# Performance work log

Hardware: AMD Instinct MI355X
Metric: run time of the kernel (lower is better)

## Reference

```python
import jax, jax.numpy as jnp
import numpy as np

K = 2            # top-k experts per sample
LOSS_COEF = 0.01


def _cv_squared(v):
    eps = 1e-10
    return jnp.var(v, ddof=1) / (jnp.mean(v) ** 2 + eps)


def setup_inputs() -> dict:
    key = jax.random.key(0)
    k1, k2, k3, k4 = jax.random.split(key, 4)
    B, S, D, O, E = 32, 512, 768, 768, 8
    return {
        "x": jax.random.normal(k1, (B, S, D), dtype=jnp.float32),
        "w_gate": jax.random.normal(k2, (D, E), dtype=jnp.float32) * 0.02,
        "weight": jax.random.normal(k3, (E, O, D), dtype=jnp.float32) * 0.02,
        "bias": jax.random.normal(k4, (E, O), dtype=jnp.float32) * 0.02,
    }


def reference(x, w_gate, weight, bias):
    # x: [B, S, D]; w_gate: [D, E]; weight: [E, O, D]; bias: [E, O]
    B = x.shape[0]
    E = w_gate.shape[1]

    # --- top-k gating (eval mode: clean logits, no noise) ---
    pooled = x.mean(-2)                       # [B, D] (moe_level != 'task'/'token')
    logits = pooled @ w_gate                  # [B, E]
    top_vals, top_idx = jax.lax.top_k(logits, min(K + 1, E))
    tk_vals, tk_idx = top_vals[:, :K], top_idx[:, :K]
    tk_gates = jax.nn.softmax(tk_vals, axis=1)            # [B, K]
    gates = jnp.zeros_like(logits).at[jnp.arange(B)[:, None], tk_idx].set(tk_gates)  # [B, E]

    load = (gates > 0).sum(0).astype(jnp.float32)          # [E]
    importance = gates.sum(0)                              # [E]
    loss = (_cv_squared(importance) + _cv_squared(load)) * LOSS_COEF

    # --- per-sample soft combination of expert weights, then batched linear ---
    # same math as sum_e gates[b,e] * weight[e] without materializing [B,E,O,D]
    expert_w = jnp.einsum('be,eoi->boi', gates, weight)    # [B, O, D]
    expert_b = jnp.einsum('be,eo->bo', gates, bias)        # [B, O]
    y = jnp.einsum('bij,bkj->bik', x, expert_w) + expert_b[:, None, :]  # [B, S, O]
    return (y, loss)
```

## Files before the change

kernel.cpp:

```cpp
#include <hip/hip_runtime.h>
#include <hip/hip_bf16.h>
#include <stdint.h>

#define B_ 32
#define S_ 512
#define D_ 768
#define O_ 768
#define E_ 8
#define YSIZE (B_ * S_ * O_)
#define BK 32

typedef __attribute__((ext_vector_type(8))) short bf16x8;
typedef __attribute__((ext_vector_type(4))) float f32x4;

static __device__ __forceinline__ unsigned short f2bf(float f) {
  union { float f; uint32_t u; } v; v.f = f;
  uint32_t u = v.u;
  uint32_t r = u + 0x7fff + ((u >> 16) & 1);
  return (unsigned short)(r >> 16);
}

static __device__ __forceinline__ void async_load16(const void* g, void* l) {
  __builtin_amdgcn_global_load_lds(
      (const __attribute__((address_space(1))) void*)g,
      (__attribute__((address_space(3))) void*)l, 16, 0, 0);
}

__global__ void k_pool_convert(const float* __restrict__ x,
                               unsigned short* __restrict__ xb,
                               float* __restrict__ psum) {
  int d  = blockIdx.x * 256 + threadIdx.x;
  int b  = blockIdx.y;
  int sc = blockIdx.z;
  const float* xp = x + ((size_t)(b * S_ + sc * 128)) * D_ + d;
  unsigned short* op = xb + ((size_t)(b * S_ + sc * 128)) * D_ + d;
  float sum = 0.f;
  #pragma unroll 8
  for (int s = 0; s < 128; ++s) {
    float v = xp[(size_t)s * D_];
    sum += v;
    op[(size_t)s * D_] = f2bf(v);
  }
  psum[(sc * B_ + b) * D_ + d] = sum;
}

__global__ __launch_bounds__(256) void k_logits(
    const float* __restrict__ psum, const float* __restrict__ w_gate,
    float* __restrict__ gates, int* __restrict__ eidx,
    float* __restrict__ gval) {
  int b = blockIdx.x;
  int tid = threadIdx.x;
  float acc[E_];
  #pragma unroll
  for (int e = 0; e < E_; ++e) acc[e] = 0.f;

  for (int d = tid; d < D_; d += 256) {
    float pooled = (psum[b * D_ + d] + psum[(B_ + b) * D_ + d] +
                    psum[(2 * B_ + b) * D_ + d] + psum[(3 * B_ + b) * D_ + d]) *
                   (1.0f / (float)S_);
    const float* wg = w_gate + d * E_;
    #pragma unroll
    for (int e = 0; e < E_; ++e) acc[e] += pooled * wg[e];
  }
  #pragma unroll
  for (int off = 32; off > 0; off >>= 1) {
    #pragma unroll
    for (int e = 0; e < E_; ++e) acc[e] += __shfl_down(acc[e], off, 64);
  }
  __shared__ float part[4][E_];
  if ((tid & 63) == 0) {
    #pragma unroll
    for (int e = 0; e < E_; ++e) part[tid >> 6][e] = acc[e];
  }
  __syncthreads();
  if (tid == 0) {
    float lg[E_];
    #pragma unroll
    for (int e = 0; e < E_; ++e)
      lg[e] = part[0][e] + part[1][e] + part[2][e] + part[3][e];
    int i0 = 0; float v0 = lg[0];
    #pragma unroll
    for (int e = 1; e < E_; ++e) { if (lg[e] > v0) { v0 = lg[e]; i0 = e; } }
    int i1 = -1; float v1 = -1e30f;
    #pragma unroll
    for (int e = 0; e < E_; ++e) {
      if (e == i0) continue;
      if (lg[e] > v1) { v1 = lg[e]; i1 = e; }
    }
    float m  = fmaxf(v0, v1);
    float x0 = expf(v0 - m), x1 = expf(v1 - m);
    float s  = x0 + x1;
    float g0 = x0 / s, g1 = x1 / s;
    #pragma unroll
    for (int e = 0; e < E_; ++e)
      gates[b * E_ + e] = (e == i0) ? g0 : ((e == i1) ? g1 : 0.f);
    eidx[b] = i0; eidx[B_ + b] = i1;
    gval[b] = g0; gval[B_ + b] = g1;
  }
}

__global__ void k_loss(const float* __restrict__ gates,
                       float* __restrict__ loss_out) {
  int tid = threadIdx.x;
  __shared__ float imp[E_], loadv[E_];
  if (tid < E_) {
    float s = 0.f, c = 0.f;
    for (int b = 0; b < B_; ++b) {
      float g = gates[b * E_ + tid];
      s += g;
      c += (g > 0.f) ? 1.f : 0.f;
    }
    imp[tid] = s; loadv[tid] = c;
  }
  __syncthreads();
  if (tid == 0) {
    double mi = 0, ml = 0;
    for (int e = 0; e < E_; ++e) { mi += imp[e]; ml += loadv[e]; }
    mi /= E_; ml /= E_;
    double vi = 0, vl = 0;
    for (int e = 0; e < E_; ++e) {
      double di = imp[e] - mi, dl = loadv[e] - ml;
      vi += di * di; vl += dl * dl;
    }
    vi /= (E_ - 1); vl /= (E_ - 1);
    double cvi = vi / (mi * mi + 1e-10);
    double cvl = vl / (ml * ml + 1e-10);
    loss_out[0] = (float)((cvi + cvl) * 0.01);
  }
}

__global__ __launch_bounds__(256) void k_moe_gemm(
    const unsigned short* __restrict__ xb, const float* __restrict__ weight,
    const int* __restrict__ eidx, const float* __restrict__ gval,
    const float* __restrict__ bias, float* __restrict__ y) {
  __shared__ unsigned short Alds[128 * BK];
  __shared__ unsigned short Blds[128 * BK];

  int b    = blockIdx.y;
  int tile = blockIdx.x;
  int st = tile & 3;
  int ot = tile >> 2;
  int s0 = st * 128, o0 = ot * 128;

  int tid  = threadIdx.x;
  int wave = tid >> 6, lane = tid & 63;
  int wm = wave & 1, wn = wave >> 1;

  int   e0 = eidx[b], e1 = eidx[B_ + b];
  float g0 = gval[b], g1 = gval[B_ + b];

  const unsigned short* Abase = xb + ((size_t)(b * S_ + s0)) * D_;
  const float* W0 = weight + (size_t)e0 * O_ * D_ + (size_t)o0 * D_;
  const float* W1 = weight + (size_t)e1 * O_ * D_ + (size_t)o0 * D_;

  int brow  = tid >> 1;
  int bhalf = tid & 1;

  f32x4 acc[4][4];
  #pragma unroll
  for (int i = 0; i < 4; ++i)
    #pragma unroll
    for (int j = 0; j < 4; ++j) acc[i][j] = (f32x4){0.f, 0.f, 0.f, 0.f};

  int a_chunk0 = wave * 2;
  int a_r = lane >> 2;
  int a_c = (lane & 3) * 8;

  for (int kk = 0; kk < D_; kk += BK) {
    __syncthreads();
    #pragma unroll
    for (int j = 0; j < 2; ++j) {
      int chunk = a_chunk0 + j;
      const unsigned short* src =
          Abase + (size_t)(chunk * 16 + a_r) * D_ + kk + a_c;
      async_load16(src, Alds + chunk * 512);
    }
    {
      const float* p0 = W0 + (size_t)brow * D_ + kk + bhalf * 16;
      const float* p1 = W1 + (size_t)brow * D_ + kk + bhalf * 16;
      uint32_t pk[8];
      #pragma unroll
      for (int i = 0; i < 4; ++i) {
        float4 u0 = ((const float4*)p0)[i];
        float4 u1 = ((const float4*)p1)[i];
        float c0 = g0 * u0.x + g1 * u1.x;
        float c1 = g0 * u0.y + g1 * u1.y;
        float c2 = g0 * u0.z + g1 * u1.z;
        float c3 = g0 * u0.w + g1 * u1.w;
        pk[i * 2 + 0] = (uint32_t)f2bf(c0) | ((uint32_t)f2bf(c1) << 16);
        pk[i * 2 + 1] = (uint32_t)f2bf(c2) | ((uint32_t)f2bf(c3) << 16);
      }
      uint32_t* dst = (uint32_t*)(Blds + brow * 32 + bhalf * 16);
      ((uint4*)dst)[0] = make_uint4(pk[0], pk[1], pk[2], pk[3]);
      ((uint4*)dst)[1] = make_uint4(pk[4], pk[5], pk[6], pk[7]);
    }
    __syncthreads();

    bf16x8 af[4], bfr[4];
    int koff = (lane >> 4) * 8;
    int r16  = lane & 15;
    #pragma unroll
    for (int mi = 0; mi < 4; ++mi)
      af[mi] = *(const bf16x8*)(Alds + (wm * 64 + mi * 16 + r16) * BK + koff);
    #pragma unroll
    for (int ni = 0; ni < 4; ++ni)
      bfr[ni] = *(const bf16x8*)(Blds + (wn * 64 + ni * 16 + r16) * BK + koff);
    #pragma unroll
    for (int mi = 0; mi < 4; ++mi)
      #pragma unroll
      for (int ni = 0; ni < 4; ++ni)
        acc[mi][ni] = __builtin_amdgcn_mfma_f32_16x16x32_bf16(
            af[mi], bfr[ni], acc[mi][ni], 0, 0, 0);
  }

  float* Y = y + ((size_t)(b * S_ + s0)) * O_ + o0;
  int col   = lane & 15;
  int rquad = (lane >> 4) * 4;
  #pragma unroll
  for (int ni = 0; ni < 4; ++ni) {
    int n = wn * 64 + ni * 16 + col;
    float cbv = g0 * bias[e0 * O_ + o0 + n] + g1 * bias[e1 * O_ + o0 + n];
    #pragma unroll
    for (int mi = 0; mi < 4; ++mi) {
      #pragma unroll
      for (int r = 0; r < 4; ++r) {
        int m = wm * 64 + mi * 16 + rquad + r;
        Y[(size_t)m * O_ + n] = acc[mi][ni][r] + cbv;
      }
    }
  }
}

extern "C" void kernel_launch(void* const* d_in, const int* in_sizes, int n_in,
                              void* d_out, int out_size, void* d_ws, size_t ws_size,
                              hipStream_t stream) {
  const float* x      = (const float*)d_in[0];
  const float* w_gate = (const float*)d_in[1];
  const float* weight = (const float*)d_in[2];
  const float* bias   = (const float*)d_in[3];
  float* y = (float*)d_out;

  float* psum  = (float*)d_ws;
  float* gates = psum + 4 * B_ * D_;
  int*   eidx  = (int*)(gates + B_ * E_);
  float* gval  = (float*)(eidx + 64);
  unsigned short* xb = (unsigned short*)((char*)d_ws + 524288);

  k_pool_convert<<<dim3(3, 32, 4), 256, 0, stream>>>(x, xb, psum);
  k_logits<<<32, 256, 0, stream>>>(psum, w_gate, gates, eidx, gval);
  k_loss<<<1, 64, 0, stream>>>(gates, y + YSIZE);
  k_moe_gemm<<<dim3(24, 32), 256, 0, stream>>>(xb, weight, eidx, gval, bias, y);
}
```

Baseline: 191.9 us.

## Precombine per-sample expert weights to bf16 and async-load both GEMM operands

Adds a k_combine kernel that reads all 8 expert weight slices once and writes a gated bf16 combined weight matrix per sample to workspace. The GEMM then loads B tiles with async global-to-LDS copies like A, instead of redundantly reading two fp32 expert slices and mixing them in every tile. Pool/convert is also split into more blocks (16 sequence chunks) for more parallelism. The cost is an extra kernel launch plus writing and rereading about 37 MB of combined weights.

Result: faster. 181.2 us (-5.6%).

```diff
diff --git a/kernel.cpp b/kernel.cpp
--- a/kernel.cpp
+++ b/kernel.cpp
@@ -9,6 +9,7 @@
 #define E_ 8
 #define YSIZE (B_ * S_ * O_)
 #define BK 32
+#define WSLICE (O_ * D_)
 
 typedef __attribute__((ext_vector_type(8))) short bf16x8;
 typedef __attribute__((ext_vector_type(4))) float f32x4;
@@ -32,11 +33,11 @@
   int d  = blockIdx.x * 256 + threadIdx.x;
   int b  = blockIdx.y;
   int sc = blockIdx.z;
-  const float* xp = x + ((size_t)(b * S_ + sc * 128)) * D_ + d;
-  unsigned short* op = xb + ((size_t)(b * S_ + sc * 128)) * D_ + d;
+  const float* xp = x + ((size_t)(b * S_ + sc * 32)) * D_ + d;
+  unsigned short* op = xb + ((size_t)(b * S_ + sc * 32)) * D_ + d;
   float sum = 0.f;
   #pragma unroll 8
-  for (int s = 0; s < 128; ++s) {
+  for (int s = 0; s < 32; ++s) {
     float v = xp[(size_t)s * D_];
     sum += v;
     op[(size_t)s * D_] = f2bf(v);
@@ -55,12 +56,13 @@
   for (int e = 0; e < E_; ++e) acc[e] = 0.f;
 
   for (int d = tid; d < D_; d += 256) {
-    float pooled = (psum[b * D_ + d] + psum[(B_ + b) * D_ + d] +
-                    psum[(2 * B_ + b) * D_ + d] + psum[(3 * B_ + b) * D_ + d]) *
-                   (1.0f / (float)S_);
+    float p = 0.f;
+    #pragma unroll
+    for (int c = 0; c < 16; ++c) p += psum[(c * B_ + b) * D_ + d];
+    p *= (1.0f / (float)S_);
     const float* wg = w_gate + d * E_;
     #pragma unroll
-    for (int e = 0; e < E_; ++e) acc[e] += pooled * wg[e];
+    for (int e = 0; e < E_; ++e) acc[e] += p * wg[e];
   }
   #pragma unroll
   for (int off = 32; off > 0; off >>= 1) {
@@ -129,8 +131,43 @@
   }
 }
 
+__global__ __launch_bounds__(256) void k_combine(
+    const float* __restrict__ weight, const float* __restrict__ gates,
+    unsigned short* __restrict__ wc) {
+  __shared__ float gsh[B_][E_];
+  int tid = threadIdx.x;
+  if (tid < B_ * E_) ((float*)gsh)[tid] = gates[tid];
+  __syncthreads();
+
+  size_t i = (size_t)blockIdx.x * 2048 + tid * 8;
+  float v[E_][8];
+  #pragma unroll
+  for (int e = 0; e < E_; ++e) {
+    float4 u0 = *(const float4*)(weight + (size_t)e * WSLICE + i);
+    float4 u1 = *(const float4*)(weight + (size_t)e * WSLICE + i + 4);
+    v[e][0] = u0.x; v[e][1] = u0.y; v[e][2] = u0.z; v[e][3] = u0.w;
+    v[e][4] = u1.x; v[e][5] = u1.y; v[e][6] = u1.z; v[e][7] = u1.w;
+  }
+  for (int b = 0; b < B_; ++b) {
+    float c[8];
+    #pragma unroll
+    for (int j = 0; j < 8; ++j) c[j] = 0.f;
+    #pragma unroll
+    for (int e = 0; e < E_; ++e) {
+      float g = gsh[b][e];
+      #pragma unroll
+      for (int j = 0; j < 8; ++j) c[j] += g * v[e][j];
+    }
+    uint32_t pk[4];
+    #pragma unroll
+    for (int j = 0; j < 4; ++j)
+      pk[j] = (uint32_t)f2bf(c[2 * j]) | ((uint32_t)f2bf(c[2 * j + 1]) << 16);
+    *(uint4*)(wc + (size_t)b * WSLICE + i) = make_uint4(pk[0], pk[1], pk[2], pk[3]);
+  }
+}
+
 __global__ __launch_bounds__(256) void k_moe_gemm(
-    const unsigned short* __restrict__ xb, const float* __restrict__ weight,
+    const unsigned short* __restrict__ xb, const unsigned short* __restrict__ wc,
     const int* __restrict__ eidx, const float* __restrict__ gval,
     const float* __restrict__ bias, float* __restrict__ y) {
   __shared__ unsigned short Alds[128 * BK];
@@ -146,15 +183,8 @@
   int wave = tid >> 6, lane = tid & 63;
   int wm = wave & 1, wn = wave >> 1;
 
-  int   e0 = eidx[b], e1 = eidx[B_ + b];
-  float g0 = gval[b], g1 = gval[B_ + b];
-
   const unsigned short* Abase = xb + ((size_t)(b * S_ + s0)) * D_;
-  const float* W0 = weight + (size_t)e0 * O_ * D_ + (size_t)o0 * D_;
-  const float* W1 = weight + (size_t)e1 * O_ * D_ + (size_t)o0 * D_;
-
-  int brow  = tid >> 1;
-  int bhalf = tid & 1;
+  const unsigned short* Bbase = wc + (size_t)b * WSLICE + (size_t)o0 * D_;
 
   f32x4 acc[4][4];
   #pragma unroll
@@ -171,28 +201,12 @@
     #pragma unroll
     for (int j = 0; j < 2; ++j) {
       int chunk = a_chunk0 + j;
-      const unsigned short* src =
+      const unsigned short* srcA =
           Abase + (size_t)(chunk * 16 + a_r) * D_ + kk + a_c;
-      async_load16(src, Alds + chunk * 512);
-    }
-    {
-      const float* p0 = W0 + (size_t)brow * D_ + kk + bhalf * 16;
-      const float* p1 = W1 + (size_t)brow * D_ + kk + bhalf * 16;
-      uint32_t pk[8];
-      #pragma unroll
-      for (int i = 0; i < 4; ++i) {
-        float4 u0 = ((const float4*)p0)[i];
-        float4 u1 = ((const float4*)p1)[i];
-        float c0 = g0 * u0.x + g1 * u1.x;
-        float c1 = g0 * u0.y + g1 * u1.y;
-        float c2 = g0 * u0.z + g1 * u1.z;
-        float c3 = g0 * u0.w + g1 * u1.w;
-        pk[i * 2 + 0] = (uint32_t)f2bf(c0) | ((uint32_t)f2bf(c1) << 16);
-        pk[i * 2 + 1] = (uint32_t)f2bf(c2) | ((uint32_t)f2bf(c3) << 16);
-      }
-      uint32_t* dst = (uint32_t*)(Blds + brow * 32 + bhalf * 16);
-      ((uint4*)dst)[0] = make_uint4(pk[0], pk[1], pk[2], pk[3]);
-      ((uint4*)dst)[1] = make_uint4(pk[4], pk[5], pk[6], pk[7]);
+      async_load16(srcA, Alds + chunk * 512);
+      const unsigned short* srcB =
+          Bbase + (size_t)(chunk * 16 + a_r) * D_ + kk + a_c;
+      async_load16(srcB, Blds + chunk * 512);
     }
     __syncthreads();
 
@@ -213,6 +227,8 @@
             af[mi], bfr[ni], acc[mi][ni], 0, 0, 0);
   }
 
+  int   e0 = eidx[b], e1 = eidx[B_ + b];
+  float g0 = gval[b], g1 = gval[B_ + b];
   float* Y = y + ((size_t)(b * S_ + s0)) * O_ + o0;
   int col   = lane & 15;
   int rquad = (lane >> 4) * 4;
@@ -241,13 +257,15 @@
   float* y = (float*)d_out;
 
   float* psum  = (float*)d_ws;
-  float* gates = psum + 4 * B_ * D_;
-  int*   eidx  = (int*)(gates + B_ * E_);
-  float* gval  = (float*)(eidx + 64);
-  unsigned short* xb = (unsigned short*)((char*)d_ws + 524288);
-
-  k_pool_convert<<<dim3(3, 32, 4), 256, 0, stream>>>(x, xb, psum);
+  float* gates = (float*)((char*)d_ws + 1572864);
+  int*   eidx  = (int*)((char*)d_ws + 1573888);
+  float* gval  = (float*)((char*)d_ws + 1574144);
+  unsigned short* xb = (unsigned short*)((char*)d_ws + 2097152);
+  unsigned short* wc = (unsigned short*)((char*)d_ws + 27262976);
+
+  k_pool_convert<<<dim3(3, 32, 16), 256, 0, stream>>>(x, xb, psum);
   k_logits<<<32, 256, 0, stream>>>(psum, w_gate, gates, eidx, gval);
   k_loss<<<1, 64, 0, stream>>>(gates, y + YSIZE);
-  k_moe_gemm<<<dim3(24, 32), 256, 0, stream>>>(xb, weight, eidx, gval, bias, y);
-}
+  k_combine<<<288, 256, 0, stream>>>(weight, gates, wc);
+  k_moe_gemm<<<dim3(24, 32), 256, 0, stream>>>(xb, wc, eidx, gval, bias, y);
+}
```
